# Performance work log

Hardware: AMD Instinct MI355X
Metric: run time of the kernel (lower is better)

## Reference

```python
import jax, jax.numpy as jnp
import numpy as np

N, C, G = 262144, 256, 1024
R = C // 4  # reduction bottleneck


def _linear_w(key, out_dim, in_dim):
    # torch.nn.Linear default init: U(-1/sqrt(in), 1/sqrt(in)), weight shape [out, in]
    bound = 1.0 / np.sqrt(in_dim)
    return jax.random.uniform(key, (out_dim, in_dim), jnp.float32, -bound, bound)


def setup_inputs() -> dict:
    key = jax.random.key(0)
    ks = jax.random.split(key, 8)
    return {
        "x": jax.random.normal(ks[0], (N, C), jnp.float32),
        "glb_w1": _linear_w(ks[1], R, C),
        "glb_a": jnp.full((1,), 0.25, jnp.float32),   # PReLU param (default init 0.25)
        "glb_w2": _linear_w(ks[2], C, R),
        "local_w1": _linear_w(ks[3], R, C),
        "local_a": jnp.full((1,), 0.25, jnp.float32),
        "local_w2": _linear_w(ks[4], C, R),
        "attn_w1": _linear_w(ks[5], R, C),
        "attn_a": jnp.full((1,), 0.25, jnp.float32),
        "attn_w2": _linear_w(ks[6], C, R),
        "batch_idx": jnp.sort(jax.random.randint(ks[7], (N,), 0, G)),
        "num_graphs": G,
    }


def _mlp(h, w1, a, w2):
    # Linear(no bias) -> PReLU -> Linear(no bias)
    z = jnp.einsum('nc,rc->nr', h, w1)
    z = jnp.where(z >= 0, z, a * z)
    return jnp.einsum('nr,cr->nc', z, w2)


def reference(x, glb_w1, glb_a, glb_w2, local_w1, local_a, local_w2,
              attn_w1, attn_a, attn_w2, batch_idx, num_graphs):
    g = _mlp(x, glb_w1, glb_a, glb_w2)                                  # [N, C]
    seg_sum = jax.ops.segment_sum(g, batch_idx, num_segments=num_graphs)  # [G, C]
    cnt = jax.ops.segment_sum(jnp.ones((x.shape[0], 1), x.dtype), batch_idx,
                              num_segments=num_graphs)                  # [G, 1]
    seg_mean = seg_sum / jnp.maximum(cnt, 1.0)  # scatter_mean (0 for empty graphs)
    x_glb = seg_mean[batch_idx]                                          # gather back [N, C]
    loc = _mlp(x, local_w1, local_a, local_w2)                           # [N, C]
    attn = _mlp(loc + x_glb, attn_w1, attn_a, attn_w2)
    return jax.nn.sigmoid(attn)
```

## Files before the change

kernel.cpp:

```cpp
#include <hip/hip_runtime.h>

typedef unsigned short u16;
typedef __attribute__((ext_vector_type(8))) short short8;
typedef __attribute__((ext_vector_type(4))) float f32x4;
typedef __attribute__((ext_vector_type(4))) unsigned short u16x4;
typedef __attribute__((ext_vector_type(2))) unsigned u32x2;

#define NN 262144
#define CC 256
#define RR 64
#define GG 1024

#define SWZ(b, n) ((b) ^ (((n) & 7) << 4))
#define SSWZ(b, r) ((b) ^ (((r) & 7) << 4))

#define XBFOFF 1249280
#define XBFSZ  ((size_t)NN * CC * 2)

static __device__ __forceinline__ u16 f2bf(float f) {
  unsigned u = __builtin_bit_cast(unsigned, f);
  u += 0x7fffu + ((u >> 16) & 1u);
  return (u16)(u >> 16);
}

static __device__ __forceinline__ unsigned cvt_pk_bf16(float lo, float hi) {
  unsigned r;
  asm("v_cvt_pk_bf16_f32 %0, %1, %2" : "=v"(r) : "v"(lo), "v"(hi));
  return r;
}

static __device__ __forceinline__ void lgkm0() {
  __asm__ volatile("s_waitcnt lgkmcnt(0)" ::: "memory");
}

static __device__ __forceinline__ void gload_lds16(const void* g, void* l) {
  __builtin_amdgcn_global_load_lds(
      (const __attribute__((address_space(1))) void*)g,
      (__attribute__((address_space(3))) void*)l, 16, 0, 0);
}

#define MFMA16(a, b, c) __builtin_amdgcn_mfma_f32_16x16x32_bf16((a), (b), (c), 0, 0, 0)

__global__ void k_prep(const float* __restrict__ a0, const float* __restrict__ a1,
                       const float* __restrict__ a2, const float* __restrict__ a3,
                       const float* __restrict__ a4, const float* __restrict__ a5,
                       u16* __restrict__ dst, float* __restrict__ zbase) {
  int bid = blockIdx.x;
  if (bid < 96) {
    int m = bid >> 4;
    const float* s = (m == 0) ? a0 : (m == 1) ? a1 : (m == 2) ? a2
                   : (m == 3) ? a3 : (m == 4) ? a4 : a5;
    int off = (((bid & 15) << 8) | threadIdx.x) << 2;
    f32x4 v = *(const f32x4*)(s + off);
    u16x4 p;
    p[0] = f2bf(v[0]); p[1] = f2bf(v[1]); p[2] = f2bf(v[2]); p[3] = f2bf(v[3]);
    *(u16x4*)(dst + m * 16384 + off) = p;
  } else {
    int idx = (bid - 96) * 256 + threadIdx.x;
    ((f32x4*)zbase)[idx] = (f32x4){0.f, 0.f, 0.f, 0.f};
  }
}

#define ZBOFF 16384

__global__ __launch_bounds__(256)
__attribute__((amdgpu_waves_per_eu(6, 6))) void k_glb(
    const float* __restrict__ x, const u16* __restrict__ wbf,
    const int* __restrict__ bidx, const float* __restrict__ pa,
    float* __restrict__ seg, int* __restrict__ cnt,
    char* __restrict__ xbf) {
  __shared__ __align__(16) char smem[20480];
  const int tid = threadIdx.x;
  const int wave = tid >> 6, lane = tid & 63;
  const int low = lane & 15, quad = lane >> 4;
  const int node0 = blockIdx.x << 5;
  const float alpha = pa[0];
  const u16* w1 = wbf;
  const u16* w2 = wbf + 16384;

  const int lbv = bidx[node0 + (lane & 31)];

  const float* xsrc = x + (size_t)node0 * CC;
  char* xtile = xbf ? (xbf + ((size_t)blockIdx.x << 14)) : nullptr;
#pragma unroll
  for (int k = 0; k < 8; k++) {
    int f = k * 1024 + tid * 4;
    f32x4 v = *(const f32x4*)(xsrc + f);
    int node = f >> 8;
    u32x2 p;
    p[0] = cvt_pk_bf16(v[0], v[1]);
    p[1] = cvt_pk_bf16(v[2], v[3]);
    int off = SWZ(node * 512 + (f & 255) * 2, node);
    *(u32x2*)(smem + off) = p;
    if (xtile) *(u32x2*)(xtile + off) = p;
  }

  if (wave == 0) {
    int cur = __shfl(lbv, 0), rl = 0;
#pragma unroll
    for (int n = 0; n < 32; n++) {
      int b = __shfl(lbv, n);
      if (b != cur) { if (lane == 0) atomicAdd(cnt + cur, rl); rl = 0; cur = b; }
      rl++;
    }
    if (lane == 0) atomicAdd(cnt + cur, rl);
  }
  __syncthreads();

  f32x4 z[2] = {};
  const u16* w1p = w1 + (wave * 16 + low) * CC;
#pragma unroll
  for (int ks = 0; ks < 8; ks++) {
    short8 wa = *(const short8*)(w1p + ks * 32 + quad * 8);
#pragma unroll
    for (int nt = 0; nt < 2; nt++) {
      int node = nt * 16 + low;
      short8 xf = *(const short8*)(smem + SWZ(node * 512 + ks * 64 + quad * 16, node));
      z[nt] = MFMA16(wa, xf, z[nt]);
    }
  }
#pragma unroll
  for (int nt = 0; nt < 2; nt++) {
    float v0 = z[nt][0], v1 = z[nt][1], v2 = z[nt][2], v3 = z[nt][3];
    v0 = v0 >= 0.f ? v0 : alpha * v0;
    v1 = v1 >= 0.f ? v1 : alpha * v1;
    v2 = v2 >= 0.f ? v2 : alpha * v2;
    v3 = v3 >= 0.f ? v3 : alpha * v3;
    int node = nt * 16 + low;
    u32x2 p;
    p[0] = cvt_pk_bf16(v0, v1);
    p[1] = cvt_pk_bf16(v2, v3);
    *(u32x2*)(smem + ZBOFF + SWZ(node * 128 + wave * 32 + quad * 8, node)) = p;
  }
  __syncthreads();

  char* slab = smem + wave * 4096;
#pragma unroll
  for (int nt = 0; nt < 2; nt++) {
    int node = nt * 16 + low;
    f32x4 g[4] = {};
#pragma unroll
    for (int ks2 = 0; ks2 < 2; ks2++) {
      short8 zf = *(const short8*)(smem + ZBOFF + SWZ(node * 128 + ks2 * 64 + quad * 16, node));
#pragma unroll
      for (int mt = 0; mt < 4; mt++) {
        short8 wa = *(const short8*)(w2 + (wave * 64 + mt * 16 + low) * RR + ks2 * 32 + quad * 8);
        g[mt] = MFMA16(wa, zf, g[mt]);
      }
    }
#pragma unroll
    for (int mt = 0; mt < 4; mt++)
      *(f32x4*)(slab + SSWZ(low * 256 + mt * 64 + quad * 16, low)) = g[mt];
    lgkm0();
    float acc = 0.f;
    int cur = __shfl(lbv, nt * 16);
#pragma unroll
    for (int n = 0; n < 16; n++) {
      int b = __shfl(lbv, nt * 16 + n);
      if (b != cur) {
        atomicAdd(seg + (size_t)cur * CC + wave * 64 + lane, acc);
        acc = 0.f; cur = b;
      }
      acc += *(const float*)(slab + SSWZ(n * 256 + lane * 4, n));
    }
    atomicAdd(seg + (size_t)cur * CC + wave * 64 + lane, acc);
    lgkm0();
  }
}

template <int USE_XBF>
__global__ __launch_bounds__(256)
__attribute__((amdgpu_waves_per_eu(6, 6))) void k_attn(
    const float* __restrict__ x, const char* __restrict__ xbf,
    const u16* __restrict__ wbf,
    const int* __restrict__ bidx, const float* __restrict__ seg,
    const int* __restrict__ cnt,
    const float* __restrict__ pal, const float* __restrict__ paa,
    float* __restrict__ out) {
  __shared__ __align__(16) char smem[20480];
  const int tid = threadIdx.x;
  const int wave = tid >> 6, lane = tid & 63;
  const int low = lane & 15, quad = lane >> 4;
  const int node0 = blockIdx.x << 5;
  const float al = pal[0], aa = paa[0];
  const u16* w1l = wbf + 2 * 16384;
  const u16* w2l = wbf + 3 * 16384;
  const u16* w1a = wbf + 4 * 16384;
  const u16* w2a = wbf + 5 * 16384;

  if (USE_XBF) {
    const char* gsrc = xbf + ((size_t)blockIdx.x << 14) + wave * 1024 + lane * 16;
    char* ldst = smem + wave * 1024 + lane * 16;
#pragma unroll
    for (int i = 0; i < 4; i++)
      gload_lds16(gsrc + i * 4096, ldst + i * 4096);
  }

  int bb[2], cc[2];
#pragma unroll
  for (int nt = 0; nt < 2; nt++) bb[nt] = bidx[node0 + nt * 16 + low];
#pragma unroll
  for (int nt = 0; nt < 2; nt++) cc[nt] = cnt[bb[nt]];

  if (!USE_XBF) {
    const float* xsrc = x + (size_t)node0 * CC;
#pragma unroll
    for (int k = 0; k < 8; k++) {
      int f = k * 1024 + tid * 4;
      f32x4 v = *(const f32x4*)(xsrc + f);
      int node = f >> 8;
      u32x2 p;
      p[0] = cvt_pk_bf16(v[0], v[1]);
      p[1] = cvt_pk_bf16(v[2], v[3]);
      *(u32x2*)(smem + SWZ(node * 512 + (f & 255) * 2, node)) = p;
    }
  }
  __syncthreads();

  f32x4 z[2] = {};
  const u16* w1p = w1l + (wave * 16 + low) * CC;
#pragma unroll
  for (int ks = 0; ks < 8; ks++) {
    short8 wa = *(const short8*)(w1p + ks * 32 + quad * 8);
#pragma unroll
    for (int nt = 0; nt < 2; nt++) {
      int node = nt * 16 + low;
      short8 xf = *(const short8*)(smem + SWZ(node * 512 + ks * 64 + quad * 16, node));
      z[nt] = MFMA16(wa, xf, z[nt]);
    }
  }
#pragma unroll
  for (int nt = 0; nt < 2; nt++) {
    float v0 = z[nt][0], v1 = z[nt][1], v2 = z[nt][2], v3 = z[nt][3];
    v0 = v0 >= 0.f ? v0 : al * v0;
    v1 = v1 >= 0.f ? v1 : al * v1;
    v2 = v2 >= 0.f ? v2 : al * v2;
    v3 = v3 >= 0.f ? v3 : al * v3;
    int node = nt * 16 + low;
    u32x2 p;
    p[0] = cvt_pk_bf16(v0, v1);
    p[1] = cvt_pk_bf16(v2, v3);
    *(u32x2*)(smem + ZBOFF + SWZ(node * 128 + wave * 32 + quad * 8, node)) = p;
  }
  __syncthreads();

#pragma unroll
  for (int nt = 0; nt < 2; nt++) {
    int node = nt * 16 + low;
    f32x4 loc[4] = {};
#pragma unroll
    for (int ks2 = 0; ks2 < 2; ks2++) {
      short8 zf = *(const short8*)(smem + ZBOFF + SWZ(node * 128 + ks2 * 64 + quad * 16, node));
#pragma unroll
      for (int mt = 0; mt < 4; mt++) {
        short8 wa = *(const short8*)(w2l + (wave * 64 + mt * 16 + low) * RR + ks2 * 32 + quad * 8);
        loc[mt] = MFMA16(wa, zf, loc[mt]);
      }
    }
    const float* srow = seg + (size_t)bb[nt] * CC + wave * 64;
    float inv = (cc[nt] > 0) ? __builtin_amdgcn_rcpf((float)cc[nt]) : 0.0f;
#pragma unroll
    for (int mt = 0; mt < 4; mt++) {
      f32x4 sv = *(const f32x4*)(srow + mt * 16 + quad * 4);
      u32x2 p;
      p[0] = cvt_pk_bf16(fmaf(sv[0], inv, loc[mt][0]),
                         fmaf(sv[1], inv, loc[mt][1]));
      p[1] = cvt_pk_bf16(fmaf(sv[2], inv, loc[mt][2]),
                         fmaf(sv[3], inv, loc[mt][3]));
      *(u32x2*)(smem + SWZ(node * 512 + wave * 128 + mt * 32 + quad * 8, node)) = p;
    }
  }
  __syncthreads();

  f32x4 z2[2] = {};
  const u16* w1pa = w1a + (wave * 16 + low) * CC;
#pragma unroll
  for (int ks = 0; ks < 8; ks++) {
    short8 wa = *(const short8*)(w1pa + ks * 32 + quad * 8);
#pragma unroll
    for (int nt = 0; nt < 2; nt++) {
      int node = nt * 16 + low;
      short8 hf = *(const short8*)(smem + SWZ(node * 512 + ks * 64 + quad * 16, node));
      z2[nt] = MFMA16(wa, hf, z2[nt]);
    }
  }
#pragma unroll
  for (int nt = 0; nt < 2; nt++) {
    float v0 = z2[nt][0], v1 = z2[nt][1], v2 = z2[nt][2], v3 = z2[nt][3];
    v0 = v0 >= 0.f ? v0 : aa * v0;
    v1 = v1 >= 0.f ? v1 : aa * v1;
    v2 = v2 >= 0.f ? v2 : aa * v2;
    v3 = v3 >= 0.f ? v3 : aa * v3;
    int node = nt * 16 + low;
    u32x2 p;
    p[0] = cvt_pk_bf16(v0, v1);
    p[1] = cvt_pk_bf16(v2, v3);
    *(u32x2*)(smem + ZBOFF + SWZ(node * 128 + wave * 32 + quad * 8, node)) = p;
  }
  __syncthreads();

#pragma unroll
  for (int nt = 0; nt < 2; nt++) {
    int node = nt * 16 + low;
    f32x4 o[4] = {};
#pragma unroll
    for (int ks2 = 0; ks2 < 2; ks2++) {
      short8 zf = *(const short8*)(smem + ZBOFF + SWZ(node * 128 + ks2 * 64 + quad * 16, node));
#pragma unroll
      for (int mt = 0; mt < 4; mt++) {
        short8 wa = *(const short8*)(w2a + (wave * 64 + mt * 16 + low) * RR + ks2 * 32 + quad * 8);
        o[mt] = MFMA16(wa, zf, o[mt]);
      }
    }
    float* orow = out + (size_t)(node0 + node) * CC + wave * 64;
#pragma unroll
    for (int mt = 0; mt < 4; mt++) {
#pragma unroll
      for (int i = 0; i < 4; i++)
        o[mt][i] = __builtin_amdgcn_rcpf(1.0f + __expf(-o[mt][i]));
      *(f32x4*)(orow + mt * 16 + quad * 4) = o[mt];
    }
  }
}

extern "C" void kernel_launch(void* const* d_in, const int* in_sizes, int n_in,
                              void* d_out, int out_size, void* d_ws, size_t ws_size,
                              hipStream_t stream) {
  (void)in_sizes; (void)n_in; (void)out_size;
  const float* x   = (const float*)d_in[0];
  const float* w1g = (const float*)d_in[1];
  const float* ag  = (const float*)d_in[2];
  const float* w2g = (const float*)d_in[3];
  const float* w1l = (const float*)d_in[4];
  const float* al  = (const float*)d_in[5];
  const float* w2l = (const float*)d_in[6];
  const float* w1a = (const float*)d_in[7];
  const float* aa  = (const float*)d_in[8];
  const float* w2a = (const float*)d_in[9];
  const int* bidx  = (const int*)d_in[10];
  float* out = (float*)d_out;

  u16* wbf   = (u16*)d_ws;
  float* seg = (float*)((char*)d_ws + 196608);
  int* cnt   = (int*)((char*)d_ws + 196608 + 1048576);
  const bool big = ws_size >= (size_t)XBFOFF + XBFSZ;
  char* xbf  = big ? ((char*)d_ws + XBFOFF) : nullptr;

  k_prep<<<353, 256, 0, stream>>>(w1g, w2g, w1l, w2l, w1a, w2a, wbf, seg);
  k_glb<<<NN / 32, 256, 0, stream>>>(x, wbf, bidx, ag, seg, cnt, xbf);
  if (big)
    k_attn<1><<<NN / 32, 256, 0, stream>>>(x, xbf, wbf, bidx, seg, cnt, al, aa, out);
  else
    k_attn<0><<<NN / 32, 256, 0, stream>>>(x, xbf, wbf, bidx, seg, cnt, al, aa, out);
}
```

Baseline: 679.3 us.

## Double attention-kernel node tile and hoist weight fragments into registers

```diff
diff --git a/kernel.cpp b/kernel.cpp
--- a/kernel.cpp
+++ b/kernel.cpp
@@ -61,10 +61,10 @@
   }
 }
 
-#define ZBOFF 16384
-
+
+#define ZB1 16384
 __global__ __launch_bounds__(256)
-__attribute__((amdgpu_waves_per_eu(6, 6))) void k_glb(
+__attribute__((amdgpu_waves_per_eu(5, 5))) void k_glb(
     const float* __restrict__ x, const u16* __restrict__ wbf,
     const int* __restrict__ bidx, const float* __restrict__ pa,
     float* __restrict__ seg, int* __restrict__ cnt,
@@ -95,6 +95,12 @@
     if (xtile) *(u32x2*)(xtile + off) = p;
   }
 
+  short8 wa1[8];
+  const u16* w1p = w1 + (wave * 16 + low) * CC;
+#pragma unroll
+  for (int ks = 0; ks < 8; ks++)
+    wa1[ks] = *(const short8*)(w1p + ks * 32 + quad * 8);
+
   if (wave == 0) {
     int cur = __shfl(lbv, 0), rl = 0;
 #pragma unroll
@@ -108,17 +114,22 @@
   __syncthreads();
 
   f32x4 z[2] = {};
-  const u16* w1p = w1 + (wave * 16 + low) * CC;
 #pragma unroll
   for (int ks = 0; ks < 8; ks++) {
-    short8 wa = *(const short8*)(w1p + ks * 32 + quad * 8);
 #pragma unroll
     for (int nt = 0; nt < 2; nt++) {
       int node = nt * 16 + low;
       short8 xf = *(const short8*)(smem + SWZ(node * 512 + ks * 64 + quad * 16, node));
-      z[nt] = MFMA16(wa, xf, z[nt]);
-    }
-  }
+      z[nt] = MFMA16(wa1[ks], xf, z[nt]);
+    }
+  }
+  short8 wa2[8];
+#pragma unroll
+  for (int ks2 = 0; ks2 < 2; ks2++)
+#pragma unroll
+    for (int mt = 0; mt < 4; mt++)
+      wa2[ks2 * 4 + mt] =
+          *(const short8*)(w2 + (wave * 64 + mt * 16 + low) * RR + ks2 * 32 + quad * 8);
 #pragma unroll
   for (int nt = 0; nt < 2; nt++) {
     float v0 = z[nt][0], v1 = z[nt][1], v2 = z[nt][2], v3 = z[nt][3];
@@ -130,7 +141,7 @@
     u32x2 p;
     p[0] = cvt_pk_bf16(v0, v1);
     p[1] = cvt_pk_bf16(v2, v3);
-    *(u32x2*)(smem + ZBOFF + SWZ(node * 128 + wave * 32 + quad * 8, node)) = p;
+    *(u32x2*)(smem + ZB1 + SWZ(node * 128 + wave * 32 + quad * 8, node)) = p;
   }
   __syncthreads();
 
@@ -141,12 +152,10 @@
     f32x4 g[4] = {};
 #pragma unroll
     for (int ks2 = 0; ks2 < 2; ks2++) {
-      short8 zf = *(const short8*)(smem + ZBOFF + SWZ(node * 128 + ks2 * 64 + quad * 16, node));
-#pragma unroll
-      for (int mt = 0; mt < 4; mt++) {
-        short8 wa = *(const short8*)(w2 + (wave * 64 + mt * 16 + low) * RR + ks2 * 32 + quad * 8);
-        g[mt] = MFMA16(wa, zf, g[mt]);
-      }
+      short8 zf = *(const short8*)(smem + ZB1 + SWZ(node * 128 + ks2 * 64 + quad * 16, node));
+#pragma unroll
+      for (int mt = 0; mt < 4; mt++)
+        g[mt] = MFMA16(wa2[ks2 * 4 + mt], zf, g[mt]);
     }
 #pragma unroll
     for (int mt = 0; mt < 4; mt++)
@@ -168,20 +177,21 @@
   }
 }
 
+#define ZB3 32768
 template <int USE_XBF>
 __global__ __launch_bounds__(256)
-__attribute__((amdgpu_waves_per_eu(6, 6))) void k_attn(
+__attribute__((amdgpu_waves_per_eu(4, 4))) void k_attn(
     const float* __restrict__ x, const char* __restrict__ xbf,
     const u16* __restrict__ wbf,
     const int* __restrict__ bidx, const float* __restrict__ seg,
     const int* __restrict__ cnt,
     const float* __restrict__ pal, const float* __restrict__ paa,
     float* __restrict__ out) {
-  __shared__ __align__(16) char smem[20480];
+  __shared__ __align__(16) char smem[40960];
   const int tid = threadIdx.x;
   const int wave = tid >> 6, lane = tid & 63;
   const int low = lane & 15, quad = lane >> 4;
-  const int node0 = blockIdx.x << 5;
+  const int node0 = blockIdx.x << 6;
   const float al = pal[0], aa = paa[0];
   const u16* w1l = wbf + 2 * 16384;
   const u16* w2l = wbf + 3 * 16384;
@@ -189,23 +199,15 @@
   const u16* w2a = wbf + 5 * 16384;
 
   if (USE_XBF) {
-    const char* gsrc = xbf + ((size_t)blockIdx.x << 14) + wave * 1024 + lane * 16;
+    const char* gsrc = xbf + ((size_t)blockIdx.x << 15) + wave * 1024 + lane * 16;
     char* ldst = smem + wave * 1024 + lane * 16;
 #pragma unroll
-    for (int i = 0; i < 4; i++)
-      gload_lds16(gsrc + i * 4096, ldst + i * 4096);
-  }
-
-  int bb[2], cc[2];
-#pragma unroll
-  for (int nt = 0; nt < 2; nt++) bb[nt] = bidx[node0 + nt * 16 + low];
-#pragma unroll
-  for (int nt = 0; nt < 2; nt++) cc[nt] = cnt[bb[nt]];
-
-  if (!USE_XBF) {
+    for (int j = 0; j < 8; j++)
+      gload_lds16(gsrc + j * 4096, ldst + j * 4096);
+  } else {
     const float* xsrc = x + (size_t)node0 * CC;
 #pragma unroll
-    for (int k = 0; k < 8; k++) {
+    for (int k = 0; k < 16; k++) {
       int f = k * 1024 + tid * 4;
       f32x4 v = *(const f32x4*)(xsrc + f);
       int node = f >> 8;
@@ -215,22 +217,40 @@
       *(u32x2*)(smem + SWZ(node * 512 + (f & 255) * 2, node)) = p;
     }
   }
-  __syncthreads();
-
-  f32x4 z[2] = {};
-  const u16* w1p = w1l + (wave * 16 + low) * CC;
+
+  int bb[4], cc2[4];
+#pragma unroll
+  for (int nt = 0; nt < 4; nt++) bb[nt] = bidx[node0 + nt * 16 + low];
+#pragma unroll
+  for (int nt = 0; nt < 4; nt++) cc2[nt] = cnt[bb[nt]];
+  short8 wa[8];
+  {
+    const u16* w1p = w1l + (wave * 16 + low) * CC;
+#pragma unroll
+    for (int ks = 0; ks < 8; ks++)
+      wa[ks] = *(const short8*)(w1p + ks * 32 + quad * 8);
+  }
+  __syncthreads();
+
+  f32x4 z[4] = {};
 #pragma unroll
   for (int ks = 0; ks < 8; ks++) {
-    short8 wa = *(const short8*)(w1p + ks * 32 + quad * 8);
-#pragma unroll
-    for (int nt = 0; nt < 2; nt++) {
+#pragma unroll
+    for (int nt = 0; nt < 4; nt++) {
       int node = nt * 16 + low;
       short8 xf = *(const short8*)(smem + SWZ(node * 512 + ks * 64 + quad * 16, node));
-      z[nt] = MFMA16(wa, xf, z[nt]);
-    }
-  }
-#pragma unroll
-  for (int nt = 0; nt < 2; nt++) {
+      z[nt] = MFMA16(wa[ks], xf, z[nt]);
+    }
+  }
+  short8 wb[8];
+#pragma unroll
+  for (int ks2 = 0; ks2 < 2; ks2++)
+#pragma unroll
+    for (int mt = 0; mt < 4; mt++)
+      wb[ks2 * 4 + mt] =
+          *(const short8*)(w2l + (wave * 64 + mt * 16 + low) * RR + ks2 * 32 + quad * 8);
+#pragma unroll
+  for (int nt = 0; nt < 4; nt++) {
     float v0 = z[nt][0], v1 = z[nt][1], v2 = z[nt][2], v3 = z[nt][3];
     v0 = v0 >= 0.f ? v0 : al * v0;
     v1 = v1 >= 0.f ? v1 : al * v1;
@@ -240,52 +260,62 @@
     u32x2 p;
     p[0] = cvt_pk_bf16(v0, v1);
     p[1] = cvt_pk_bf16(v2, v3);
-    *(u32x2*)(smem + ZBOFF + SWZ(node * 128 + wave * 32 + quad * 8, node)) = p;
-  }
-  __syncthreads();
-
-#pragma unroll
-  for (int nt = 0; nt < 2; nt++) {
-    int node = nt * 16 + low;
+    *(u32x2*)(smem + ZB3 + SWZ(node * 128 + wave * 32 + quad * 8, node)) = p;
+  }
+  __syncthreads();
+
+#pragma unroll
+  for (int nt = 0; nt < 4; nt++) {
+    int node = nt * 16 + low;
+    const float* srow = seg + (size_t)bb[nt] * CC + wave * 64;
+    f32x4 sv[4];
+#pragma unroll
+    for (int mt = 0; mt < 4; mt++) sv[mt] = *(const f32x4*)(srow + mt * 16 + quad * 4);
     f32x4 loc[4] = {};
 #pragma unroll
     for (int ks2 = 0; ks2 < 2; ks2++) {
-      short8 zf = *(const short8*)(smem + ZBOFF + SWZ(node * 128 + ks2 * 64 + quad * 16, node));
-#pragma unroll
-      for (int mt = 0; mt < 4; mt++) {
-        short8 wa = *(const short8*)(w2l + (wave * 64 + mt * 16 + low) * RR + ks2 * 32 + quad * 8);
-        loc[mt] = MFMA16(wa, zf, loc[mt]);
-      }
-    }
-    const float* srow = seg + (size_t)bb[nt] * CC + wave * 64;
-    float inv = (cc[nt] > 0) ? __builtin_amdgcn_rcpf((float)cc[nt]) : 0.0f;
+      short8 zf = *(const short8*)(smem + ZB3 + SWZ(node * 128 + ks2 * 64 + quad * 16, node));
+#pragma unroll
+      for (int mt = 0; mt < 4; mt++)
+        loc[mt] = MFMA16(wb[ks2 * 4 + mt], zf, loc[mt]);
+    }
+    float inv = (cc2[nt] > 0) ? __builtin_amdgcn_rcpf((float)cc2[nt]) : 0.0f;
 #pragma unroll
     for (int mt = 0; mt < 4; mt++) {
-      f32x4 sv = *(const f32x4*)(srow + mt * 16 + quad * 4);
       u32x2 p;
-      p[0] = cvt_pk_bf16(fmaf(sv[0], inv, loc[mt][0]),
-                         fmaf(sv[1], inv, loc[mt][1]));
-      p[1] = cvt_pk_bf16(fmaf(sv[2], inv, loc[mt][2]),
-                         fmaf(sv[3], inv, loc[mt][3]));
+      p[0] = cvt_pk_bf16(fmaf(sv[mt][0], inv, loc[mt][0]),
+                         fmaf(sv[mt][1], inv, loc[mt][1]));
+      p[1] = cvt_pk_bf16(fmaf(sv[mt][2], inv, loc[mt][2]),
+                         fmaf(sv[mt][3], inv, loc[mt][3]));
       *(u32x2*)(smem + SWZ(node * 512 + wave * 128 + mt * 32 + quad * 8, node)) = p;
     }
   }
-  __syncthreads();
-
-  f32x4 z2[2] = {};
-  const u16* w1pa = w1a + (wave * 16 + low) * CC;
+  {
+    const u16* w1p = w1a + (wave * 16 + low) * CC;
+#pragma unroll
+    for (int ks = 0; ks < 8; ks++)
+      wa[ks] = *(const short8*)(w1p + ks * 32 + quad * 8);
+  }
+  __syncthreads();
+
+  f32x4 z2[4] = {};
 #pragma unroll
   for (int ks = 0; ks < 8; ks++) {
-    short8 wa = *(const short8*)(w1pa + ks * 32 + quad * 8);
-#pragma unroll
-    for (int nt = 0; nt < 2; nt++) {
+#pragma unroll
+    for (int nt = 0; nt < 4; nt++) {
       int node = nt * 16 + low;
       short8 hf = *(const short8*)(smem + SWZ(node * 512 + ks * 64 + quad * 16, node));
-      z2[nt] = MFMA16(wa, hf, z2[nt]);
-    }
-  }
-#pragma unroll
-  for (int nt = 0; nt < 2; nt++) {
+      z2[nt] = MFMA16(wa[ks], hf, z2[nt]);
+    }
+  }
+#pragma unroll
+  for (int ks2 = 0; ks2 < 2; ks2++)
+#pragma unroll
+    for (int mt = 0; mt < 4; mt++)
+      wb[ks2 * 4 + mt] =
+          *(const short8*)(w2a + (wave * 64 + mt * 16 + low) * RR + ks2 * 32 + quad * 8);
+#pragma unroll
+  for (int nt = 0; nt < 4; nt++) {
     float v0 = z2[nt][0], v1 = z2[nt][1], v2 = z2[nt][2], v3 = z2[nt][3];
     v0 = v0 >= 0.f ? v0 : aa * v0;
     v1 = v1 >= 0.f ? v1 : aa * v1;
@@ -295,22 +325,20 @@
     u32x2 p;
     p[0] = cvt_pk_bf16(v0, v1);
     p[1] = cvt_pk_bf16(v2, v3);
-    *(u32x2*)(smem + ZBOFF + SWZ(node * 128 + wave * 32 + quad * 8, node)) = p;
-  }
-  __syncthreads();
-
-#pragma unroll
-  for (int nt = 0; nt < 2; nt++) {
+    *(u32x2*)(smem + ZB3 + SWZ(node * 128 + wave * 32 + quad * 8, node)) = p;
+  }
+  __syncthreads();
+
+#pragma unroll
+  for (int nt = 0; nt < 4; nt++) {
     int node = nt * 16 + low;
     f32x4 o[4] = {};
 #pragma unroll
     for (int ks2 = 0; ks2 < 2; ks2++) {
-      short8 zf = *(const short8*)(smem + ZBOFF + SWZ(node * 128 + ks2 * 64 + quad * 16, node));
-#pragma unroll
-      for (int mt = 0; mt < 4; mt++) {
-        short8 wa = *(const short8*)(w2a + (wave * 64 + mt * 16 + low) * RR + ks2 * 32 + quad * 8);
-        o[mt] = MFMA16(wa, zf, o[mt]);
-      }
+      short8 zf = *(const short8*)(smem + ZB3 + SWZ(node * 128 + ks2 * 64 + quad * 16, node));
+#pragma unroll
+      for (int mt = 0; mt < 4; mt++)
+        o[mt] = MFMA16(wb[ks2 * 4 + mt], zf, o[mt]);
     }
     float* orow = out + (size_t)(node0 + node) * CC + wave * 64;
 #pragma unroll
@@ -343,13 +371,12 @@
   u16* wbf   = (u16*)d_ws;
   float* seg = (float*)((char*)d_ws + 196608);
   int* cnt   = (int*)((char*)d_ws + 196608 + 1048576);
-  const bool big = ws_size >= (size_t)XBFOFF + XBFSZ;
-  char* xbf  = big ? ((char*)d_ws + XBFOFF) : nullptr;
+  char* xbf  = (ws_size >= (size_t)XBFOFF + XBFSZ) ? ((char*)d_ws + XBFOFF) : nullptr;
 
   k_prep<<<353, 256, 0, stream>>>(w1g, w2g, w1l, w2l, w1a, w2a, wbf, seg);
   k_glb<<<NN / 32, 256, 0, stream>>>(x, wbf, bidx, ag, seg, cnt, xbf);
-  if (big)
-    k_attn<1><<<NN / 32, 256, 0, stream>>>(x, xbf, wbf, bidx, seg, cnt, al, aa, out);
+  if (xbf)
+    k_attn<1><<<NN / 64, 256, 0, stream>>>(x, xbf, wbf, bidx, seg, cnt, al, aa, out);
   else
-    k_attn<0><<<NN / 32, 256, 0, stream>>>(x, xbf, wbf, bidx, seg, cnt, al, aa, out);
-}
+    k_attn<0><<<NN / 64, 256, 0, stream>>>(x, xbf, wbf, bidx, seg, cnt, al, aa, out);
+}
```

Result: faster. 587.5 us (-13.5%).
